# Performance work log

Measured on AMD Instinct MI355X. Metric: run time of the kernel, lower is better.

The kernel has to match this reference:

```python
import jax, jax.numpy as jnp
import numpy as np

IN, H, B = 2048, 2048, 8192


def setup_inputs() -> dict:
    key = jax.random.key(0)
    ks = jax.random.split(key, 10)
    k = float(np.sqrt(1.0 / H))
    u = lambda kk, shape: jax.random.uniform(kk, shape, jnp.float32, -k, k)
    return {
        "x_t": jax.random.normal(ks[0], (B, IN), jnp.float32),
        "h_t1": jax.random.normal(ks[1], (B, H), jnp.float32),
        "c_t1": jax.random.normal(ks[2], (B, H), jnp.float32),
        # fused input-to-hidden weights, gate order [f, i, g, o]
        "W_i": u(ks[3], (IN, 4 * H)),
        "b_i": u(ks[4], (4 * H,)),
        # fused hidden-to-hidden weights, gate order [f, i, g, o]
        "W_h": u(ks[5], (H, 4 * H)),
        "b_h": u(ks[6], (4 * H,)),
    }


def reference(x_t, h_t1, c_t1, W_i, b_i, W_h, b_h):
    # Two fused GEMMs replace the 8 separate nn.Linear calls (same math).
    gates = (x_t @ W_i + b_i) + (h_t1 @ W_h + b_h)  # [B, 4H]
    f_pre, i_pre, g_pre, o_pre = jnp.split(gates, 4, axis=-1)
    f_t = jax.nn.sigmoid(f_pre)
    i_t = jax.nn.sigmoid(i_pre)
    g_t = jnp.tanh(g_pre)
    o_t = jax.nn.sigmoid(o_pre)
    c_t = f_t * c_t1 + i_t * g_t
    h_t = o_t * jnp.tanh(c_t)
    return (h_t, h_t, c_t)
```

## Files before the change

### kernel.cpp

```cpp
#include <hip/hip_runtime.h>
#include <hip/hip_bf16.h>
#include <stdint.h>


typedef short bf16x8 __attribute__((ext_vector_type(8)));
typedef float f32x4 __attribute__((ext_vector_type(4)));
typedef float f32x16 __attribute__((ext_vector_type(16)));

typedef const __attribute__((address_space(1))) void* gptr_as1;
typedef __attribute__((address_space(3))) void* lptr_as3;

__device__ __forceinline__ void g2lds16(const void* g, void* l) {
  __builtin_amdgcn_global_load_lds((gptr_as1)g, (lptr_as3)l, 16, 0, 0);
}

__device__ __forceinline__ short f2bs(float x) {
  __hip_bfloat16 h = __float2bfloat16(x);
  return *reinterpret_cast<short*>(&h);
}

__global__ __launch_bounds__(256) void transpose_w(const float* __restrict__ Wi,
                                                   const float* __restrict__ Wh,
                                                   __hip_bfloat16* __restrict__ Wt) {
  __shared__ float tile[64][65];
  const int nt = blockIdx.x * 64;
  const int kt = blockIdx.y * 64;
  const float* src = (kt < 2048) ? (Wi + (size_t)kt * 8192)
                                 : (Wh + (size_t)(kt - 2048) * 8192);
  const int t = threadIdx.x;
#pragma unroll
  for (int i = 0; i < 4; ++i) {
    const int c = i * 256 + t;
    const int kr = c >> 4, cc = c & 15;
    const float4 v = *(const float4*)(src + (size_t)kr * 8192 + nt + cc * 4);
    tile[kr][cc * 4 + 0] = v.x;
    tile[kr][cc * 4 + 1] = v.y;
    tile[kr][cc * 4 + 2] = v.z;
    tile[kr][cc * 4 + 3] = v.w;
  }
  __syncthreads();
#pragma unroll
  for (int i = 0; i < 2; ++i) {
    const int c = i * 256 + t;
    const int nr = c >> 3, ck = c & 7;
    bf16x8 o;
#pragma unroll
    for (int j = 0; j < 8; ++j) o[j] = f2bs(tile[ck * 8 + j][nr]);
    *(bf16x8*)(Wt + (size_t)(nt + nr) * 4096 + kt + ck * 8) = o;
  }
}

__global__ __launch_bounds__(256) void convert_a(const float* __restrict__ X,
                                                 const float* __restrict__ Hp,
                                                 __hip_bfloat16* __restrict__ Abf) {
  const int idx = blockIdx.x * 256 + threadIdx.x;
  const int m = idx >> 9, g = idx & 511;
  const float* src = (g < 256) ? (X + (size_t)m * 2048 + g * 8)
                               : (Hp + (size_t)m * 2048 + (g - 256) * 8);
  const float4 a = *(const float4*)src;
  const float4 b = *(const float4*)(src + 4);
  bf16x8 o;
  o[0] = f2bs(a.x); o[1] = f2bs(a.y); o[2] = f2bs(a.z); o[3] = f2bs(a.w);
  o[4] = f2bs(b.x); o[5] = f2bs(b.y); o[6] = f2bs(b.z); o[7] = f2bs(b.w);
  *(bf16x8*)(Abf + (size_t)m * 4096 + g * 8) = o;
}

__global__ __launch_bounds__(256, 2) void lstm_fused(
    const __hip_bfloat16* __restrict__ Abf,
    const __hip_bfloat16* __restrict__ Wt,
    const float* __restrict__ Cp,
    const float* __restrict__ bi,
    const float* __restrict__ bh,
    float* __restrict__ out)
{
  __shared__ __align__(16) __hip_bfloat16 As[8192];
  __shared__ __align__(16) __hip_bfloat16 Bs[4096];
  const int t  = threadIdx.x;
  const int m0 = blockIdx.x * 256;
  const int j0 = blockIdx.y * 32;

  const __hip_bfloat16* ga[4]; __hip_bfloat16* la[4];
#pragma unroll
  for (int i = 0; i < 4; ++i) {
    const int c = i * 256 + t;
    const int row = c >> 2, pos = c & 3, qg = pos ^ (row & 3);
    ga[i] = Abf + (size_t)(m0 + row) * 4096 + qg * 8;
    la[i] = As + c * 8;
  }
  const __hip_bfloat16* gb[2]; __hip_bfloat16* lb[2];
#pragma unroll
  for (int i = 0; i < 2; ++i) {
    const int c = i * 256 + t;
    const int row = c >> 2, pos = c & 3, qg = pos ^ (row & 3);
    const int n = (row >> 5) * 2048 + j0 + (row & 31);
    gb[i] = Wt + (size_t)n * 4096 + qg * 8;
    lb[i] = Bs + c * 8;
  }

  const int w = t >> 6, lane = t & 63;
  const int lm = lane & 31, lk = lane >> 5;

  int aoff[2][2], boff[4][2];
#pragma unroll
  for (int tm = 0; tm < 2; ++tm) {
    const int ra = w * 64 + tm * 32 + lm;
#pragma unroll
    for (int kk = 0; kk < 2; ++kk)
      aoff[tm][kk] = ra * 32 + (((lk + 2 * kk)) ^ (ra & 3)) * 8;
  }
#pragma unroll
  for (int g = 0; g < 4; ++g) {
    const int rb = g * 32 + lm;
#pragma unroll
    for (int kk = 0; kk < 2; ++kk)
      boff[g][kk] = rb * 32 + (((lk + 2 * kk)) ^ (rb & 3)) * 8;
  }

  f32x16 acc[2][4];
#pragma unroll
  for (int a = 0; a < 2; ++a)
#pragma unroll
    for (int b = 0; b < 4; ++b)
#pragma unroll
      for (int r = 0; r < 16; ++r) acc[a][b][r] = 0.f;

  for (int k0 = 0; k0 < 4096; k0 += 32) {
    __syncthreads();
#pragma unroll
    for (int i = 0; i < 4; ++i) g2lds16(ga[i] + k0, la[i]);
#pragma unroll
    for (int i = 0; i < 2; ++i) g2lds16(gb[i] + k0, lb[i]);
    __syncthreads();
#pragma unroll
    for (int kk = 0; kk < 2; ++kk) {
      bf16x8 af[2], bv[4];
      af[0] = *(const bf16x8*)(As + aoff[0][kk]);
      af[1] = *(const bf16x8*)(As + aoff[1][kk]);
#pragma unroll
      for (int g = 0; g < 4; ++g) bv[g] = *(const bf16x8*)(Bs + boff[g][kk]);
#pragma unroll
      for (int tm = 0; tm < 2; ++tm)
#pragma unroll
        for (int g = 0; g < 4; ++g)
          acc[tm][g] = __builtin_amdgcn_mfma_f32_32x32x16_bf16(af[tm], bv[g],
                                                               acc[tm][g], 0, 0, 0);
    }
  }

  const int j = j0 + lm;
  float bsum[4];
#pragma unroll
  for (int g = 0; g < 4; ++g) bsum[g] = bi[g * 2048 + j] + bh[g * 2048 + j];

#pragma unroll
  for (int tm = 0; tm < 2; ++tm) {
#pragma unroll
    for (int r = 0; r < 16; ++r) {
      const int rowcd = (r & 3) + 8 * (r >> 2) + 4 * lk;
      const int m = m0 + w * 64 + tm * 32 + rowcd;
      const size_t off = (size_t)m * 2048 + j;
      const float fp = acc[tm][0][r] + bsum[0];
      const float ip = acc[tm][1][r] + bsum[1];
      const float gp = acc[tm][2][r] + bsum[2];
      const float op = acc[tm][3][r] + bsum[3];
      const float ft = 1.f / (1.f + __expf(-fp));
      const float it = 1.f / (1.f + __expf(-ip));
      const float gt = 1.f - 2.f / (1.f + __expf(2.f * gp));
      const float ot = 1.f / (1.f + __expf(-op));
      const float ct = ft * Cp[off] + it * gt;
      const float ht = ot * (1.f - 2.f / (1.f + __expf(2.f * ct)));
      out[off] = ht;
      out[16777216 + off] = ht;
      out[33554432 + off] = ct;
    }
  }
}

__global__ __launch_bounds__(256) void lstm_fused_f32a(
    const float* __restrict__ X, const float* __restrict__ Hp,
    const float* __restrict__ Cp, const __hip_bfloat16* __restrict__ Wt,
    const float* __restrict__ bi, const float* __restrict__ bh,
    float* __restrict__ out)
{
  __shared__ __align__(16) float As[4096];
  __shared__ __align__(16) __hip_bfloat16 Bs[4096];
  const int t  = threadIdx.x;
  const int m0 = blockIdx.x * 128;
  const int j0 = blockIdx.y * 32;

  const float* gax[4]; const float* gah[4]; float* la[4];
#pragma unroll
  for (int i = 0; i < 4; ++i) {
    const int c = i * 256 + t;
    const int row = c >> 3, pos = c & 7;
    const int qg = pos ^ (row & 7);
    gax[i] = X  + (size_t)(m0 + row) * 2048 + qg * 4;
    gah[i] = Hp + (size_t)(m0 + row) * 2048 + qg * 4;
    la[i]  = As + c * 4;
  }
  const __hip_bfloat16* gb[2]; __hip_bfloat16* lb[2];
#pragma unroll
  for (int i = 0; i < 2; ++i) {
    const int c = i * 256 + t;
    const int row = c >> 2, pos = c & 3;
    const int qg = pos ^ ((row >> 1) & 3);
    const int n = (row >> 5) * 2048 + j0 + (row & 31);
    gb[i] = Wt + (size_t)n * 4096 + qg * 8;
    lb[i] = Bs + c * 8;
  }

  const int w = t >> 6, lane = t & 63;
  const int wr = w >> 1, wc = w & 1;
  const int lq = lane >> 4, ln = lane & 15;

  f32x4 acc[4][4];
#pragma unroll
  for (int a = 0; a < 4; ++a)
#pragma unroll
    for (int b = 0; b < 4; ++b) acc[a][b] = (f32x4){0.f, 0.f, 0.f, 0.f};

  for (int k0 = 0; k0 < 4096; k0 += 32) {
    __syncthreads();
    if (k0 < 2048) {
#pragma unroll
      for (int i = 0; i < 4; ++i) g2lds16(gax[i] + k0, la[i]);
    } else {
#pragma unroll
      for (int i = 0; i < 4; ++i) g2lds16(gah[i] + (k0 - 2048), la[i]);
    }
#pragma unroll
    for (int i = 0; i < 2; ++i) g2lds16(gb[i] + k0, lb[i]);
    __syncthreads();

    bf16x8 af[4], bv[4];
#pragma unroll
    for (int tm = 0; tm < 4; ++tm) {
      const int m = wr * 64 + tm * 16 + ln;
      const f32x4 f0 = *(const f32x4*)(As + m * 32 + ((lq * 2)     ^ (m & 7)) * 4);
      const f32x4 f1 = *(const f32x4*)(As + m * 32 + ((lq * 2 + 1) ^ (m & 7)) * 4);
      bf16x8 v;
      v[0] = f2bs(f0[0]); v[1] = f2bs(f0[1]); v[2] = f2bs(f0[2]); v[3] = f2bs(f0[3]);
      v[4] = f2bs(f1[0]); v[5] = f2bs(f1[1]); v[6] = f2bs(f1[2]); v[7] = f2bs(f1[3]);
      af[tm] = v;
    }
#pragma unroll
    for (int g = 0; g < 4; ++g) {
      const int row = g * 32 + wc * 16 + ln;
      bv[g] = *(const bf16x8*)(Bs + row * 32 + (lq ^ ((row >> 1) & 3)) * 8);
    }
#pragma unroll
    for (int tm = 0; tm < 4; ++tm)
#pragma unroll
      for (int g = 0; g < 4; ++g)
        acc[tm][g] = __builtin_amdgcn_mfma_f32_16x16x32_bf16(af[tm], bv[g],
                                                             acc[tm][g], 0, 0, 0);
  }

  const int jg = j0 + wc * 16 + ln;
  float bsum[4];
#pragma unroll
  for (int g = 0; g < 4; ++g) bsum[g] = bi[g * 2048 + jg] + bh[g * 2048 + jg];

#pragma unroll
  for (int tm = 0; tm < 4; ++tm) {
#pragma unroll
    for (int r = 0; r < 4; ++r) {
      const int m = m0 + wr * 64 + tm * 16 + lq * 4 + r;
      const size_t off = (size_t)m * 2048 + jg;
      const float fp = acc[tm][0][r] + bsum[0];
      const float ip = acc[tm][1][r] + bsum[1];
      const float gp = acc[tm][2][r] + bsum[2];
      const float op = acc[tm][3][r] + bsum[3];
      const float ft = 1.f / (1.f + __expf(-fp));
      const float it = 1.f / (1.f + __expf(-ip));
      const float gt = 1.f - 2.f / (1.f + __expf(2.f * gp));
      const float ot = 1.f / (1.f + __expf(-op));
      const float ct = ft * Cp[off] + it * gt;
      const float ht = ot * (1.f - 2.f / (1.f + __expf(2.f * ct)));
      out[off] = ht;
      out[16777216 + off] = ht;
      out[33554432 + off] = ct;
    }
  }
}

extern "C" void kernel_launch(void* const* d_in, const int* in_sizes, int n_in,
                              void* d_out, int out_size, void* d_ws, size_t ws_size,
                              hipStream_t stream) {
  const float* X  = (const float*)d_in[0];
  const float* Hp = (const float*)d_in[1];
  const float* Cp = (const float*)d_in[2];
  const float* Wi = (const float*)d_in[3];
  const float* bi = (const float*)d_in[4];
  const float* Wh = (const float*)d_in[5];
  const float* bh = (const float*)d_in[6];
  float* out = (float*)d_out;
  __hip_bfloat16* Wt = (__hip_bfloat16*)d_ws;

  transpose_w<<<dim3(128, 64), dim3(256), 0, stream>>>(Wi, Wh, Wt);

  if (ws_size >= (size_t)134217728) {
    __hip_bfloat16* Abf = (__hip_bfloat16*)d_ws + 33554432;
    convert_a<<<16384, 256, 0, stream>>>(X, Hp, Abf);
    lstm_fused<<<dim3(32, 64), 256, 0, stream>>>(Abf, Wt, Cp, bi, bh, out);
  } else {
    lstm_fused_f32a<<<dim3(64, 64), 256, 0, stream>>>(X, Hp, Cp, Wt, bi, bh, out);
  }
}
```

Measured before the change: 1.075 ms.

## Pre-tile A and W into k-step blocks and double-buffer LDS in GEMM

The weight transpose and activation conversion kernels now write bf16 data in a tile-major layout, so each 32-wide k step of a block's A and B tiles is one contiguous chunk that the GEMM loads with simple linear global-to-LDS copies. The main kernel double-buffers LDS, issuing the next stage's loads before computing on the current one, with one barrier per iteration instead of two. This aims to improve load coalescing, drop address arithmetic and overlap memory with MFMA work. The cost is doubled LDS use (48KB per block), which may limit occupancy at two blocks per CU, and the unswizzled LDS reads may hit bank conflicts. The convert kernel's per-thread 128B strided reads may coalesce poorly.

```diff
diff --git a/kernel.cpp b/kernel.cpp
--- a/kernel.cpp
+++ b/kernel.cpp
@@ -19,9 +19,9 @@
   return *reinterpret_cast<short*>(&h);
 }
 
-__global__ __launch_bounds__(256) void transpose_w(const float* __restrict__ Wi,
-                                                   const float* __restrict__ Wh,
-                                                   __hip_bfloat16* __restrict__ Wt) {
+__global__ __launch_bounds__(256) void transpose_w_tiled(
+    const float* __restrict__ Wi, const float* __restrict__ Wh,
+    __hip_bfloat16* __restrict__ Wt) {
   __shared__ float tile[64][65];
   const int nt = blockIdx.x * 64;
   const int kt = blockIdx.y * 64;
@@ -39,30 +39,48 @@
     tile[kr][cc * 4 + 3] = v.w;
   }
   __syncthreads();
+  const int g  = nt >> 11;
+  const int nb = nt & 2047;
 #pragma unroll
   for (int i = 0; i < 2; ++i) {
     const int c = i * 256 + t;
-    const int nr = c >> 3, ck = c & 7;
+    const int ck = c >> 6, nr = c & 63;
     bf16x8 o;
 #pragma unroll
     for (int j = 0; j < 8; ++j) o[j] = f2bs(tile[ck * 8 + j][nr]);
-    *(bf16x8*)(Wt + (size_t)(nt + nr) * 4096 + kt + ck * 8) = o;
+    const int nl = nb + nr;
+    const int jb = nl >> 5, jj = nl & 31;
+    const int s  = (kt >> 5) + (ck >> 2);
+    const int kc = ck & 3;
+    const int r  = g * 32 + jj;
+    *(bf16x8*)(Wt + (((size_t)(jb * 128 + s) * 4 + kc) * 128 + r) * 8) = o;
   }
 }
 
 __global__ __launch_bounds__(256) void convert_a(const float* __restrict__ X,
                                                  const float* __restrict__ Hp,
                                                  __hip_bfloat16* __restrict__ Abf) {
-  const int idx = blockIdx.x * 256 + threadIdx.x;
-  const int m = idx >> 9, g = idx & 511;
-  const float* src = (g < 256) ? (X + (size_t)m * 2048 + g * 8)
-                               : (Hp + (size_t)m * 2048 + (g - 256) * 8);
-  const float4 a = *(const float4*)src;
-  const float4 b = *(const float4*)(src + 4);
-  bf16x8 o;
-  o[0] = f2bs(a.x); o[1] = f2bs(a.y); o[2] = f2bs(a.z); o[3] = f2bs(a.w);
-  o[4] = f2bs(b.x); o[5] = f2bs(b.y); o[6] = f2bs(b.z); o[7] = f2bs(b.w);
-  *(bf16x8*)(Abf + (size_t)m * 4096 + g * 8) = o;
+  const int b = blockIdx.x;
+  const int p = b >> 7, s = b & 127;
+  const int t = threadIdx.x;
+  const int m = p * 256 + t;
+  const float* src = (s < 64) ? (X + (size_t)m * 2048 + s * 32)
+                              : (Hp + (size_t)m * 2048 + (s - 64) * 32);
+  float v[32];
+#pragma unroll
+  for (int i = 0; i < 8; ++i) {
+    const float4 f = *(const float4*)(src + i * 4);
+    v[i * 4 + 0] = f.x; v[i * 4 + 1] = f.y;
+    v[i * 4 + 2] = f.z; v[i * 4 + 3] = f.w;
+  }
+  __hip_bfloat16* dst = Abf + ((size_t)(p * 128 + s) * 1024) * 8 + t * 8;
+#pragma unroll
+  for (int kc = 0; kc < 4; ++kc) {
+    bf16x8 o;
+#pragma unroll
+    for (int j = 0; j < 8; ++j) o[j] = f2bs(v[kc * 8 + j]);
+    *(bf16x8*)(dst + kc * 2048) = o;
+  }
 }
 
 __global__ __launch_bounds__(256, 2) void lstm_fused(
@@ -73,49 +91,19 @@
     const float* __restrict__ bh,
     float* __restrict__ out)
 {
-  __shared__ __align__(16) __hip_bfloat16 As[8192];
-  __shared__ __align__(16) __hip_bfloat16 Bs[4096];
-  const int t  = threadIdx.x;
-  const int m0 = blockIdx.x * 256;
-  const int j0 = blockIdx.y * 32;
-
-  const __hip_bfloat16* ga[4]; __hip_bfloat16* la[4];
-#pragma unroll
-  for (int i = 0; i < 4; ++i) {
-    const int c = i * 256 + t;
-    const int row = c >> 2, pos = c & 3, qg = pos ^ (row & 3);
-    ga[i] = Abf + (size_t)(m0 + row) * 4096 + qg * 8;
-    la[i] = As + c * 8;
-  }
-  const __hip_bfloat16* gb[2]; __hip_bfloat16* lb[2];
-#pragma unroll
-  for (int i = 0; i < 2; ++i) {
-    const int c = i * 256 + t;
-    const int row = c >> 2, pos = c & 3, qg = pos ^ (row & 3);
-    const int n = (row >> 5) * 2048 + j0 + (row & 31);
-    gb[i] = Wt + (size_t)n * 4096 + qg * 8;
-    lb[i] = Bs + c * 8;
-  }
+  __shared__ __align__(16) __hip_bfloat16 As[2][8192];
+  __shared__ __align__(16) __hip_bfloat16 Bs[2][4096];
+  const int t   = threadIdx.x;
+  const int p   = blockIdx.x;
+  const int jbl = blockIdx.y;
+  const int m0 = p * 256, j0 = jbl * 32;
+
+  const __hip_bfloat16* Ab = Abf + (size_t)p   * (128 * 8192);
+  const __hip_bfloat16* Bb = Wt  + (size_t)jbl * (128 * 4096);
 
   const int w = t >> 6, lane = t & 63;
   const int lm = lane & 31, lk = lane >> 5;
 
-  int aoff[2][2], boff[4][2];
-#pragma unroll
-  for (int tm = 0; tm < 2; ++tm) {
-    const int ra = w * 64 + tm * 32 + lm;
-#pragma unroll
-    for (int kk = 0; kk < 2; ++kk)
-      aoff[tm][kk] = ra * 32 + (((lk + 2 * kk)) ^ (ra & 3)) * 8;
-  }
-#pragma unroll
-  for (int g = 0; g < 4; ++g) {
-    const int rb = g * 32 + lm;
-#pragma unroll
-    for (int kk = 0; kk < 2; ++kk)
-      boff[g][kk] = rb * 32 + (((lk + 2 * kk)) ^ (rb & 3)) * 8;
-  }
-
   f32x16 acc[2][4];
 #pragma unroll
   for (int a = 0; a < 2; ++a)
@@ -124,20 +112,33 @@
 #pragma unroll
       for (int r = 0; r < 16; ++r) acc[a][b][r] = 0.f;
 
-  for (int k0 = 0; k0 < 4096; k0 += 32) {
-    __syncthreads();
-#pragma unroll
-    for (int i = 0; i < 4; ++i) g2lds16(ga[i] + k0, la[i]);
-#pragma unroll
-    for (int i = 0; i < 2; ++i) g2lds16(gb[i] + k0, lb[i]);
-    __syncthreads();
+  auto stage = [&](int buf, int s) {
+    const __hip_bfloat16* as = Ab + (size_t)s * 8192 + t * 8;
+    __hip_bfloat16* la = &As[buf][t * 8];
+#pragma unroll
+    for (int i = 0; i < 4; ++i) g2lds16(as + i * 2048, la + i * 2048);
+    const __hip_bfloat16* bs = Bb + (size_t)s * 4096 + t * 8;
+    __hip_bfloat16* lb = &Bs[buf][t * 8];
+#pragma unroll
+    for (int i = 0; i < 2; ++i) g2lds16(bs + i * 2048, lb + i * 2048);
+  };
+
+  stage(0, 0);
+  __syncthreads();
+  int cur = 0;
+  for (int s = 0; s < 128; ++s) {
+    if (s < 127) stage(cur ^ 1, s + 1);
 #pragma unroll
     for (int kk = 0; kk < 2; ++kk) {
+      const int kcA = (2 * kk + lk) * 256;
+      const int kcB = (2 * kk + lk) * 128;
       bf16x8 af[2], bv[4];
-      af[0] = *(const bf16x8*)(As + aoff[0][kk]);
-      af[1] = *(const bf16x8*)(As + aoff[1][kk]);
-#pragma unroll
-      for (int g = 0; g < 4; ++g) bv[g] = *(const bf16x8*)(Bs + boff[g][kk]);
+#pragma unroll
+      for (int tm = 0; tm < 2; ++tm)
+        af[tm] = *(const bf16x8*)(&As[cur][(kcA + w * 64 + tm * 32 + lm) * 8]);
+#pragma unroll
+      for (int g = 0; g < 4; ++g)
+        bv[g] = *(const bf16x8*)(&Bs[cur][(kcB + g * 32 + lm) * 8]);
 #pragma unroll
       for (int tm = 0; tm < 2; ++tm)
 #pragma unroll
@@ -145,6 +146,8 @@
           acc[tm][g] = __builtin_amdgcn_mfma_f32_32x32x16_bf16(af[tm], bv[g],
                                                                acc[tm][g], 0, 0, 0);
     }
+    __syncthreads();
+    cur ^= 1;
   }
 
   const int j = j0 + lm;
@@ -176,6 +179,37 @@
   }
 }
 
+__global__ __launch_bounds__(256) void transpose_w_nk(const float* __restrict__ Wi,
+                                                      const float* __restrict__ Wh,
+                                                      __hip_bfloat16* __restrict__ Wt) {
+  __shared__ float tile[64][65];
+  const int nt = blockIdx.x * 64;
+  const int kt = blockIdx.y * 64;
+  const float* src = (kt < 2048) ? (Wi + (size_t)kt * 8192)
+                                 : (Wh + (size_t)(kt - 2048) * 8192);
+  const int t = threadIdx.x;
+#pragma unroll
+  for (int i = 0; i < 4; ++i) {
+    const int c = i * 256 + t;
+    const int kr = c >> 4, cc = c & 15;
+    const float4 v = *(const float4*)(src + (size_t)kr * 8192 + nt + cc * 4);
+    tile[kr][cc * 4 + 0] = v.x;
+    tile[kr][cc * 4 + 1] = v.y;
+    tile[kr][cc * 4 + 2] = v.z;
+    tile[kr][cc * 4 + 3] = v.w;
+  }
+  __syncthreads();
+#pragma unroll
+  for (int i = 0; i < 2; ++i) {
+    const int c = i * 256 + t;
+    const int nr = c >> 3, ck = c & 7;
+    bf16x8 o;
+#pragma unroll
+    for (int j = 0; j < 8; ++j) o[j] = f2bs(tile[ck * 8 + j][nr]);
+    *(bf16x8*)(Wt + (size_t)(nt + nr) * 4096 + kt + ck * 8) = o;
+  }
+}
+
 __global__ __launch_bounds__(256) void lstm_fused_f32a(
     const float* __restrict__ X, const float* __restrict__ Hp,
     const float* __restrict__ Cp, const __hip_bfloat16* __restrict__ Wt,
@@ -297,13 +331,13 @@
   float* out = (float*)d_out;
   __hip_bfloat16* Wt = (__hip_bfloat16*)d_ws;
 
-  transpose_w<<<dim3(128, 64), dim3(256), 0, stream>>>(Wi, Wh, Wt);
-
   if (ws_size >= (size_t)134217728) {
     __hip_bfloat16* Abf = (__hip_bfloat16*)d_ws + 33554432;
-    convert_a<<<16384, 256, 0, stream>>>(X, Hp, Abf);
+    transpose_w_tiled<<<dim3(128, 64), dim3(256), 0, stream>>>(Wi, Wh, Wt);
+    convert_a<<<4096, 256, 0, stream>>>(X, Hp, Abf);
     lstm_fused<<<dim3(32, 64), 256, 0, stream>>>(Abf, Wt, Cp, bi, bh, out);
   } else {
+    transpose_w_nk<<<dim3(128, 64), dim3(256), 0, stream>>>(Wi, Wh, Wt);
     lstm_fused_f32a<<<dim3(64, 64), 256, 0, stream>>>(X, Hp, Cp, Wt, bi, bh, out);
   }
 }
```

Result: faster. 1.029 ms (-4.3%).
